# Kernel tuning notes

Hardware: AMD Instinct MI355X
Metric: run time of the kernel (lower is better)

The kernel has to match this reference:

```python
import jax, jax.numpy as jnp
import numpy as np

N_NODES = 100000
N_EDGES = 1600000
IN_CH = 128
HID = 128
OUT_CH = 2
NUM_GRAPHS = 512


def _mlp_params(key, d_in, d_out):
    k1, k2 = jax.random.split(key)
    s1 = 1.0 / np.sqrt(d_in)
    s2 = 1.0 / np.sqrt(d_out)
    return (jax.random.uniform(k1, (d_in, d_out), jnp.float32, -s1, s1),
            jnp.zeros((d_out,), jnp.float32),
            jax.random.uniform(k2, (d_out, d_out), jnp.float32, -s2, s2),
            jnp.zeros((d_out,), jnp.float32))


def setup_inputs() -> dict:
    key = jax.random.key(0)
    ks = jax.random.split(key, 8)
    x = jax.random.normal(ks[0], (N_NODES, IN_CH), jnp.float32)
    edge_index = jax.random.randint(ks[1], (2, N_EDGES), 0, N_NODES, jnp.int64)
    batch = jnp.sort(jax.random.randint(ks[2], (N_NODES,), 0, NUM_GRAPHS, jnp.int64))
    w1_0, b1_0, w2_0, b2_0 = _mlp_params(ks[3], IN_CH, HID)
    w1_1, b1_1, w2_1, b2_1 = _mlp_params(ks[4], HID, HID)
    w1_2, b1_2, w2_2, b2_2 = _mlp_params(ks[5], HID, HID)
    s = 1.0 / np.sqrt(HID)
    w_lin = jax.random.uniform(ks[6], (HID, OUT_CH), jnp.float32, -s, s)
    b_lin = jnp.zeros((OUT_CH,), jnp.float32)
    return {"x": x, "edge_index": edge_index, "batch": batch,
            "w1_0": w1_0, "b1_0": b1_0, "w2_0": w2_0, "b2_0": b2_0,
            "w1_1": w1_1, "b1_1": b1_1, "w2_1": w2_1, "b2_1": b2_1,
            "w1_2": w1_2, "b1_2": b1_2, "w2_2": w2_2, "b2_2": b2_2,
            "w_lin": w_lin, "b_lin": b_lin}


def _gin_conv(x, src, dst, w1, b1, w2, b2):
    # GINConv with eps=0: MLP(x + sum_{j in N(i)} x_j)
    agg = jax.ops.segment_sum(x[src], dst, num_segments=N_NODES)  # [N, d]
    h = x + agg
    h = jax.nn.relu(h @ w1 + b1)
    return h @ w2 + b2


def reference(x, edge_index, batch,
              w1_0, b1_0, w2_0, b2_0,
              w1_1, b1_1, w2_1, b2_1,
              w1_2, b1_2, w2_2, b2_2,
              w_lin, b_lin):
    src, dst = edge_index[0], edge_index[1]
    h = _gin_conv(x, src, dst, w1_0, b1_0, w2_0, b2_0)
    h = jax.nn.relu(h)
    h = jax.nn.relu(_gin_conv(h, src, dst, w1_1, b1_1, w2_1, b2_1))
    h = jax.nn.relu(h)  # forward applies relu twice after GIN1
    h = _gin_conv(h, src, dst, w1_2, b1_2, w2_2, b2_2)
    # global mean pool per graph
    sums = jax.ops.segment_sum(h, batch, num_segments=NUM_GRAPHS)  # [G, d]
    counts = jax.ops.segment_sum(jnp.ones((N_NODES,), h.dtype), batch,
                                 num_segments=NUM_GRAPHS)
    pooled = sums / jnp.maximum(counts, 1.0)[:, None]
    # dropout is identity in eval mode
    return pooled @ w_lin + b_lin  # [G, OUT_CH]
```

## Files before the change

### kernel.cpp

```cpp
#include <hip/hip_runtime.h>
#include <hip/hip_bf16.h>

#define N_NODES   100000
#define N_EDGES   1600000
#define IN_CH     128
#define HID       128
#define OUT_CH    2
#define NUM_GRAPHS 512

#define BKT_SHIFT 9
#define NB2 ((N_NODES + 511) >> BKT_SHIFT)
#define PB  200
#define CHUNK (N_EDGES / PB)

typedef __attribute__((ext_vector_type(8))) short bf16x8;
typedef __attribute__((ext_vector_type(4))) float f32x4;
typedef unsigned int uint32;
typedef unsigned long long uint64;

static __device__ __forceinline__ float b2f(uint32 b) {
    return __uint_as_float(b << 16);
}
static __device__ __forceinline__ unsigned short f2b(float f) {
    uint32 u = __float_as_uint(f);
    u += 0x7fffu + ((u >> 16) & 1u);
    return (unsigned short)(u >> 16);
}
static __device__ __forceinline__ void acc8(float* a, int4 v) {
    uint32 x;
    x = (uint32)v.x; a[0] += __uint_as_float(x << 16); a[1] += __uint_as_float(x & 0xffff0000u);
    x = (uint32)v.y; a[2] += __uint_as_float(x << 16); a[3] += __uint_as_float(x & 0xffff0000u);
    x = (uint32)v.z; a[4] += __uint_as_float(x << 16); a[5] += __uint_as_float(x & 0xffff0000u);
    x = (uint32)v.w; a[6] += __uint_as_float(x << 16); a[7] += __uint_as_float(x & 0xffff0000u);
}

__global__ void k_cast(const float* __restrict__ x, unsigned short* __restrict__ h) {
    int i = blockIdx.x * blockDim.x + threadIdx.x;
    int base = i * 4;
    float4 v = *(const float4*)(x + base);
    ushort4 o;
    o.x = f2b(v.x); o.y = f2b(v.y); o.z = f2b(v.z); o.w = f2b(v.w);
    *(ushort4*)(h + base) = o;
}

__global__ void k_wprep(const float* w0, const float* w1, const float* w2,
                        const float* w3, const float* w4, const float* w5,
                        unsigned short* __restrict__ wt) {
    const float* ws[6] = {w0, w1, w2, w3, w4, w5};
    const float* w = ws[blockIdx.x];
    unsigned short* o = wt + blockIdx.x * 16384;
    for (int i = threadIdx.x; i < 16384; i += 256) {
        int k = i >> 7, n = i & 127;
        o[n * 128 + k] = f2b(w[i]);
    }
}

__global__ void k_p1(const int* __restrict__ dst, int* __restrict__ histG) {
    __shared__ int h[NB2];
    int t = threadIdx.x, blk = blockIdx.x;
    for (int i = t; i < NB2; i += 512) h[i] = 0;
    __syncthreads();
    int base = blk * CHUNK;
    for (int i = t; i < CHUNK; i += 512)
        atomicAdd(&h[dst[base + i] >> BKT_SHIFT], 1);
    __syncthreads();
    for (int i = t; i < NB2; i += 512) histG[i * PB + blk] = h[i];
}

__global__ void k_scan1(const int* __restrict__ in, int* __restrict__ out,
                        int* __restrict__ bsum, int n) {
    __shared__ int sm[256];
    int b = blockIdx.x, t = threadIdx.x;
    int base = b * 1024 + t * 4;
    int v0 = 0, v1 = 0, v2 = 0, v3 = 0;
    if (base + 3 < n) {
        int4 q = *(const int4*)(in + base);
        v0 = q.x; v1 = q.y; v2 = q.z; v3 = q.w;
    } else {
        if (base + 0 < n) v0 = in[base + 0];
        if (base + 1 < n) v1 = in[base + 1];
        if (base + 2 < n) v2 = in[base + 2];
        if (base + 3 < n) v3 = in[base + 3];
    }
    int s = v0 + v1 + v2 + v3;
    sm[t] = s;
    __syncthreads();
    for (int off = 1; off < 256; off <<= 1) {
        int u = (t >= off) ? sm[t - off] : 0;
        __syncthreads();
        sm[t] += u;
        __syncthreads();
    }
    int p = (t == 0) ? 0 : sm[t - 1];
    int o0 = p, o1 = p + v0, o2 = o1 + v1, o3 = o2 + v2;
    if (base + 3 < n) {
        *(int4*)(out + base) = make_int4(o0, o1, o2, o3);
    } else {
        if (base + 0 < n) out[base + 0] = o0;
        if (base + 1 < n) out[base + 1] = o1;
        if (base + 2 < n) out[base + 2] = o2;
        if (base + 3 < n) out[base + 3] = o3;
    }
    if (t == 255) bsum[b] = s + ((t == 0) ? 0 : sm[t - 1]);
}

__global__ void k_scan2(int* __restrict__ bsum, int nb) {
    __shared__ int sm[128];
    int t = threadIdx.x;
    int v = (t < nb) ? bsum[t] : 0;
    sm[t] = v;
    __syncthreads();
    for (int off = 1; off < 128; off <<= 1) {
        int u = (t >= off) ? sm[t - off] : 0;
        __syncthreads();
        sm[t] += u;
        __syncthreads();
    }
    int p = (t == 0) ? 0 : sm[t - 1];
    if (t < nb) bsum[t] = p;
}

__global__ void k_scan3b(int* __restrict__ out, const int* __restrict__ bsum, int n) {
    int b = blockIdx.x, t = threadIdx.x;
    int base = b * 1024 + t * 4;
    int add = bsum[b];
    if (base + 3 < n) {
        int4 q = *(const int4*)(out + base);
        q.x += add; q.y += add; q.z += add; q.w += add;
        *(int4*)(out + base) = q;
    } else {
        for (int j = 0; j < 4; ++j)
            if (base + j < n) out[base + j] += add;
    }
}

__global__ void k_p3(const int* __restrict__ ei, const int* __restrict__ baseG,
                     uint64* __restrict__ ebuf) {
    __shared__ int cur[NB2];
    int t = threadIdx.x, blk = blockIdx.x;
    for (int i = t; i < NB2; i += 512) cur[i] = baseG[i * PB + blk];
    __syncthreads();
    int base = blk * CHUNK;
    for (int i = t; i < CHUNK; i += 512) {
        int e = base + i;
        int src = ei[e];
        int dst = ei[N_EDGES + e];
        int pos = atomicAdd(&cur[dst >> BKT_SHIFT], 1);
        ebuf[pos] = ((uint64)(uint32)dst << 32) | (uint32)src;
    }
}

__global__ void k_p4(const uint64* __restrict__ ebuf, const int* __restrict__ baseG,
                     int* __restrict__ off, int* __restrict__ csr) {
    __shared__ int ldeg[512];
    __shared__ int lscan[512];
    __shared__ int lcur[512];
    int b = blockIdx.x, t = threadIdx.x;
    int node0 = b << BKT_SHIFT;
    int nn = min(512, N_NODES - node0);
    int e0 = baseG[b * PB];
    int e1 = (b == NB2 - 1) ? N_EDGES : baseG[(b + 1) * PB];
    ldeg[t] = 0;
    __syncthreads();
    for (int e = e0 + t; e < e1; e += 512) {
        int dst = (int)(ebuf[e] >> 32);
        atomicAdd(&ldeg[dst - node0], 1);
    }
    __syncthreads();
    lscan[t] = ldeg[t];
    __syncthreads();
    for (int o = 1; o < 512; o <<= 1) {
        int v = (t >= o) ? lscan[t - o] : 0;
        __syncthreads();
        lscan[t] += v;
        __syncthreads();
    }
    int excl = (t == 0) ? 0 : lscan[t - 1];
    lcur[t] = e0 + excl;
    if (t < nn) off[node0 + t] = e0 + excl;
    if (b == NB2 - 1 && t == 0) off[N_NODES] = N_EDGES;
    __syncthreads();
    for (int e = e0 + t; e < e1; e += 512) {
        uint64 pr = ebuf[e];
        int dst = (int)(pr >> 32);
        int pos = atomicAdd(&lcur[dst - node0], 1);
        csr[pos] = (int)(pr & 0xffffffffu);
    }
}

__global__ void k_goff(const int* __restrict__ batch, int* __restrict__ goff) {
    int g = blockIdx.x * blockDim.x + threadIdx.x;
    if (g > NUM_GRAPHS) return;
    int lo = 0, hi = N_NODES;
    while (lo < hi) {
        int mid = (lo + hi) >> 1;
        if (batch[mid] < g) lo = mid + 1; else hi = mid;
    }
    goff[g] = lo;
}

__global__ void k_agg(const unsigned short* __restrict__ h,
                      const int* __restrict__ off, const int* __restrict__ csr,
                      unsigned short* __restrict__ hs) {
    int wid = (blockIdx.x * 256 + threadIdx.x) >> 6;
    int lane = threadIdx.x & 63;
    if (wid >= N_NODES) return;
    int g = lane >> 4, sub = lane & 15;
    int e0 = off[wid], e1 = off[wid + 1];
    float a[8] = {0.f, 0.f, 0.f, 0.f, 0.f, 0.f, 0.f, 0.f};
    int e = e0 + g;
    for (; e + 4 < e1; e += 8) {
        int s0 = csr[e];
        int s1 = csr[e + 4];
        int4 v0 = *(const int4*)(h + (size_t)s0 * 128 + sub * 8);
        int4 v1 = *(const int4*)(h + (size_t)s1 * 128 + sub * 8);
        acc8(a, v0);
        acc8(a, v1);
    }
    if (e < e1) {
        int s0 = csr[e];
        int4 v0 = *(const int4*)(h + (size_t)s0 * 128 + sub * 8);
        acc8(a, v0);
    }
#pragma unroll
    for (int j = 0; j < 8; ++j) {
        a[j] += __shfl_xor(a[j], 16);
        a[j] += __shfl_xor(a[j], 32);
    }
    if (g == 0) {
        int4 sv = *(const int4*)(h + (size_t)wid * 128 + sub * 8);
        acc8(a, sv);
        int4 o;
        o.x = (int)((uint32)f2b(a[0]) | ((uint32)f2b(a[1]) << 16));
        o.y = (int)((uint32)f2b(a[2]) | ((uint32)f2b(a[3]) << 16));
        o.z = (int)((uint32)f2b(a[4]) | ((uint32)f2b(a[5]) << 16));
        o.w = (int)((uint32)f2b(a[6]) | ((uint32)f2b(a[7]) << 16));
        *(int4*)(hs + (size_t)wid * 128 + sub * 8) = o;
    }
}

template<int OUTER_RELU>
__global__ void k_mlp(const unsigned short* __restrict__ hs,
                      const unsigned short* __restrict__ w1t, const float* __restrict__ b1,
                      const unsigned short* __restrict__ w2t, const float* __restrict__ b2,
                      unsigned short* __restrict__ ho) {
    __shared__ unsigned short T[128 * 128];
    int tid = threadIdx.x;
    int lane = tid & 63, wave = tid >> 6;
    int l15 = lane & 15, l4 = lane >> 4;
    int row0 = blockIdx.x * 128;
    int wn0 = wave * 32;

    bf16x8 w1f[2][4], w2f[2][4];
#pragma unroll
    for (int nt = 0; nt < 2; ++nt)
#pragma unroll
        for (int k = 0; k < 4; ++k) {
            int o = (wn0 + nt * 16 + l15) * 128 + k * 32 + l4 * 8;
            w1f[nt][k] = *(const bf16x8*)(w1t + o);
            w2f[nt][k] = *(const bf16x8*)(w2t + o);
        }
    float bias1[2] = { b1[wn0 + l15], b1[wn0 + 16 + l15] };
    float bias2[2] = { b2[wn0 + l15], b2[wn0 + 16 + l15] };

#pragma unroll
    for (int mt = 0; mt < 8; ++mt) {
        int arow = row0 + mt * 16 + l15;
        if (arow >= N_NODES) arow = N_NODES - 1;
        const unsigned short* ap = hs + (size_t)arow * 128 + l4 * 8;
        bf16x8 a0 = *(const bf16x8*)(ap);
        bf16x8 a1 = *(const bf16x8*)(ap + 32);
        bf16x8 a2 = *(const bf16x8*)(ap + 64);
        bf16x8 a3 = *(const bf16x8*)(ap + 96);
#pragma unroll
        for (int nt = 0; nt < 2; ++nt) {
            f32x4 acc = {0.f, 0.f, 0.f, 0.f};
            acc = __builtin_amdgcn_mfma_f32_16x16x32_bf16(a0, w1f[nt][0], acc, 0, 0, 0);
            acc = __builtin_amdgcn_mfma_f32_16x16x32_bf16(a1, w1f[nt][1], acc, 0, 0, 0);
            acc = __builtin_amdgcn_mfma_f32_16x16x32_bf16(a2, w1f[nt][2], acc, 0, 0, 0);
            acc = __builtin_amdgcn_mfma_f32_16x16x32_bf16(a3, w1f[nt][3], acc, 0, 0, 0);
#pragma unroll
            for (int j = 0; j < 4; ++j) {
                float v = fmaxf(acc[j] + bias1[nt], 0.f);
                int trow = mt * 16 + l4 * 4 + j;
                int tcol = wn0 + nt * 16 + l15;
                int byte = (trow * 256 + tcol * 2) ^ ((trow & 7) << 4);
                *(unsigned short*)((char*)T + byte) = f2b(v);
            }
        }
    }
    __syncthreads();

#pragma unroll
    for (int mt = 0; mt < 8; ++mt) {
        int trow = mt * 16 + l15;
        int sw = (trow & 7) << 4;
        int rb = trow * 256 + l4 * 16;
        bf16x8 t0 = *(const bf16x8*)((const char*)T + ((rb + 0)   ^ sw));
        bf16x8 t1 = *(const bf16x8*)((const char*)T + ((rb + 64)  ^ sw));
        bf16x8 t2 = *(const bf16x8*)((const char*)T + ((rb + 128) ^ sw));
        bf16x8 t3 = *(const bf16x8*)((const char*)T + ((rb + 192) ^ sw));
        __syncthreads();
#pragma unroll
        for (int nt = 0; nt < 2; ++nt) {
            f32x4 acc = {0.f, 0.f, 0.f, 0.f};
            acc = __builtin_amdgcn_mfma_f32_16x16x32_bf16(t0, w2f[nt][0], acc, 0, 0, 0);
            acc = __builtin_amdgcn_mfma_f32_16x16x32_bf16(t1, w2f[nt][1], acc, 0, 0, 0);
            acc = __builtin_amdgcn_mfma_f32_16x16x32_bf16(t2, w2f[nt][2], acc, 0, 0, 0);
            acc = __builtin_amdgcn_mfma_f32_16x16x32_bf16(t3, w2f[nt][3], acc, 0, 0, 0);
#pragma unroll
            for (int j = 0; j < 4; ++j) {
                float v = acc[j] + bias2[nt];
                if (OUTER_RELU) v = fmaxf(v, 0.f);
                int orow = mt * 16 + l4 * 4 + j;
                int ocol = wn0 + nt * 16 + l15;
                int byte = (orow * 256 + ocol * 2) ^ ((orow & 7) << 4);
                *(unsigned short*)((char*)T + byte) = f2b(v);
            }
        }
    }
    __syncthreads();

    for (int c = tid; c < 2048; c += 256) {
        int r = c >> 4, cc = c & 15;
        int byte = (r * 256 + cc * 16) ^ ((r & 7) << 4);
        int4 v = *(const int4*)((const char*)T + byte);
        int gr = row0 + r;
        if (gr < N_NODES)
            *(int4*)(ho + (size_t)gr * 128 + cc * 8) = v;
    }
}

__global__ void k_pool(const unsigned short* __restrict__ h,
                       const int* __restrict__ goff,
                       const float* __restrict__ wl, const float* __restrict__ bl,
                       float* __restrict__ out) {
    int g = blockIdx.x;
    int lane = threadIdx.x;
    int e0 = goff[g], e1 = goff[g + 1];
    int c2 = lane << 1;
    float s0 = 0.f, s1 = 0.f;
    int r = e0;
    for (; r + 1 < e1; r += 2) {
        uint32 v0 = *(const uint32*)(h + (size_t)r * 128 + c2);
        uint32 v1 = *(const uint32*)(h + (size_t)(r + 1) * 128 + c2);
        s0 += b2f(v0 & 0xffffu) + b2f(v1 & 0xffffu);
        s1 += b2f(v0 >> 16) + b2f(v1 >> 16);
    }
    if (r < e1) {
        uint32 v = *(const uint32*)(h + (size_t)r * 128 + c2);
        s0 += b2f(v & 0xffffu);
        s1 += b2f(v >> 16);
    }
    float inv = 1.f / fmaxf((float)(e1 - e0), 1.f);
    s0 *= inv; s1 *= inv;
    float o0 = s0 * wl[c2 * 2]     + s1 * wl[(c2 + 1) * 2];
    float o1 = s0 * wl[c2 * 2 + 1] + s1 * wl[(c2 + 1) * 2 + 1];
#pragma unroll
    for (int d = 32; d; d >>= 1) {
        o0 += __shfl_down(o0, d);
        o1 += __shfl_down(o1, d);
    }
    if (lane == 0) {
        out[g * 2]     = o0 + bl[0];
        out[g * 2 + 1] = o1 + bl[1];
    }
}

extern "C" void kernel_launch(void* const* d_in, const int* in_sizes, int n_in,
                              void* d_out, int out_size, void* d_ws, size_t ws_size,
                              hipStream_t stream) {
    const float* x     = (const float*)d_in[0];
    const int*   ei    = (const int*)d_in[1];
    const int*   batch = (const int*)d_in[2];
    const float* w1[3] = {(const float*)d_in[3],  (const float*)d_in[7],  (const float*)d_in[11]};
    const float* b1[3] = {(const float*)d_in[4],  (const float*)d_in[8],  (const float*)d_in[12]};
    const float* w2[3] = {(const float*)d_in[5],  (const float*)d_in[9],  (const float*)d_in[13]};
    const float* b2[3] = {(const float*)d_in[6],  (const float*)d_in[10], (const float*)d_in[14]};
    const float* wl    = (const float*)d_in[15];
    const float* bl    = (const float*)d_in[16];

    char* p = (char*)d_ws;
    auto alloc = [&](size_t bytes) {
        char* r = p;
        p += (bytes + 255) & ~(size_t)255;
        return r;
    };
    int* off    = (int*)alloc((size_t)(N_NODES + 1) * 4);
    int* goff   = (int*)alloc((size_t)(NUM_GRAPHS + 1) * 4);
    int* histG  = (int*)alloc((size_t)(NB2 * PB) * 4);
    int* baseG  = (int*)alloc((size_t)(NB2 * PB + 1) * 4);
    int* bsum   = (int*)alloc((size_t)128 * 4);
    int* csr    = (int*)alloc((size_t)N_EDGES * 4);
    unsigned short* wts = (unsigned short*)alloc((size_t)6 * 16384 * 2);
    unsigned short* hA  = (unsigned short*)alloc((size_t)N_NODES * 128 * 2);
    unsigned short* hS  = (unsigned short*)alloc((size_t)N_NODES * 128 * 2);
    unsigned short* hB  = (unsigned short*)alloc((size_t)N_NODES * 128 * 2);
    uint64* ebuf = (uint64*)hS;

    k_cast<<<(N_NODES * IN_CH / 4 + 255) / 256, 256, 0, stream>>>(x, hA);
    k_wprep<<<6, 256, 0, stream>>>(w1[0], w2[0], w1[1], w2[1], w1[2], w2[2], wts);

    k_p1<<<PB, 512, 0, stream>>>(ei + N_EDGES, histG);
    const int SCAN_N = NB2 * PB;
    const int SCAN_BLOCKS = (SCAN_N + 1023) / 1024;
    k_scan1<<<SCAN_BLOCKS, 256, 0, stream>>>(histG, baseG, bsum, SCAN_N);
    k_scan2<<<1, 128, 0, stream>>>(bsum, SCAN_BLOCKS);
    k_scan3b<<<SCAN_BLOCKS, 256, 0, stream>>>(baseG, bsum, SCAN_N);
    k_p3<<<PB, 512, 0, stream>>>(ei, baseG, ebuf);
    k_p4<<<NB2, 512, 0, stream>>>(ebuf, baseG, off, csr);

    k_goff<<<3, 256, 0, stream>>>(batch, goff);

    unsigned short* wt1[3] = {wts,             wts + 2 * 16384, wts + 4 * 16384};
    unsigned short* wt2[3] = {wts + 1 * 16384, wts + 3 * 16384, wts + 5 * 16384};

    const int AGG_GRID = N_NODES / 4;
    const int MLP_GRID = (N_NODES + 127) / 128;

    k_agg<<<AGG_GRID, 256, 0, stream>>>(hA, off, csr, hS);
    k_mlp<1><<<MLP_GRID, 256, 0, stream>>>(hS, wt1[0], b1[0], wt2[0], b2[0], hB);
    k_agg<<<AGG_GRID, 256, 0, stream>>>(hB, off, csr, hS);
    k_mlp<1><<<MLP_GRID, 256, 0, stream>>>(hS, wt1[1], b1[1], wt2[1], b2[1], hA);
    k_agg<<<AGG_GRID, 256, 0, stream>>>(hA, off, csr, hS);
    k_mlp<0><<<MLP_GRID, 256, 0, stream>>>(hS, wt1[2], b1[2], wt2[2], b2[2], hB);

    k_pool<<<NUM_GRAPHS, 64, 0, stream>>>(hB, goff, wl, bl, (float*)d_out);
}
```

Baseline: 398.1 us.

## Fuse preprocessing launches, unroll gather and pool loops, halve MLP row tile

Merges the cast, weight-prep and histogram kernels into one launch, and folds the graph-offset search into the edge-scatter kernel as extra blocks, removing several launches. The aggregation loop gains a 4-way unrolled stage to keep more neighbour gathers in flight, and the pool loop is unrolled 4-way. The MLP kernel processes 64 rows per block instead of 128, doubling the grid and halving shared memory use to raise occupancy, at the cost of reloading the weight fragments more often. The histogram blocks now run with 256 threads instead of 512.

```diff
diff --git a/kernel.cpp b/kernel.cpp
--- a/kernel.cpp
+++ b/kernel.cpp
@@ -13,6 +13,8 @@
 #define PB  200
 #define CHUNK (N_EDGES / PB)
 
+#define NCAST (N_NODES * IN_CH / 4 / 256)
+
 typedef __attribute__((ext_vector_type(8))) short bf16x8;
 typedef __attribute__((ext_vector_type(4))) float f32x4;
 typedef unsigned int uint32;
@@ -34,37 +36,38 @@
     x = (uint32)v.w; a[6] += __uint_as_float(x << 16); a[7] += __uint_as_float(x & 0xffff0000u);
 }
 
-__global__ void k_cast(const float* __restrict__ x, unsigned short* __restrict__ h) {
-    int i = blockIdx.x * blockDim.x + threadIdx.x;
-    int base = i * 4;
-    float4 v = *(const float4*)(x + base);
-    ushort4 o;
-    o.x = f2b(v.x); o.y = f2b(v.y); o.z = f2b(v.z); o.w = f2b(v.w);
-    *(ushort4*)(h + base) = o;
-}
-
-__global__ void k_wprep(const float* w0, const float* w1, const float* w2,
+__global__ void k_front(const float* __restrict__ x, unsigned short* __restrict__ h,
+                        const float* w0, const float* w1, const float* w2,
                         const float* w3, const float* w4, const float* w5,
-                        unsigned short* __restrict__ wt) {
-    const float* ws[6] = {w0, w1, w2, w3, w4, w5};
-    const float* w = ws[blockIdx.x];
-    unsigned short* o = wt + blockIdx.x * 16384;
-    for (int i = threadIdx.x; i < 16384; i += 256) {
-        int k = i >> 7, n = i & 127;
-        o[n * 128 + k] = f2b(w[i]);
-    }
-}
-
-__global__ void k_p1(const int* __restrict__ dst, int* __restrict__ histG) {
-    __shared__ int h[NB2];
-    int t = threadIdx.x, blk = blockIdx.x;
-    for (int i = t; i < NB2; i += 512) h[i] = 0;
-    __syncthreads();
-    int base = blk * CHUNK;
-    for (int i = t; i < CHUNK; i += 512)
-        atomicAdd(&h[dst[base + i] >> BKT_SHIFT], 1);
-    __syncthreads();
-    for (int i = t; i < NB2; i += 512) histG[i * PB + blk] = h[i];
+                        unsigned short* __restrict__ wt,
+                        const int* __restrict__ dst, int* __restrict__ histG) {
+    __shared__ int hist[NB2];
+    int bid = blockIdx.x, t = threadIdx.x;
+    if (bid < NCAST) {
+        int base = (bid * 256 + t) * 4;
+        float4 v = *(const float4*)(x + base);
+        ushort4 o;
+        o.x = f2b(v.x); o.y = f2b(v.y); o.z = f2b(v.z); o.w = f2b(v.w);
+        *(ushort4*)(h + base) = o;
+    } else if (bid < NCAST + 6) {
+        const float* ws[6] = {w0, w1, w2, w3, w4, w5};
+        int wi = bid - NCAST;
+        const float* w = ws[wi];
+        unsigned short* o = wt + wi * 16384;
+        for (int i = t; i < 16384; i += 256) {
+            int k = i >> 7, n = i & 127;
+            o[n * 128 + k] = f2b(w[i]);
+        }
+    } else {
+        int blk = bid - NCAST - 6;
+        for (int i = t; i < NB2; i += 256) hist[i] = 0;
+        __syncthreads();
+        int base = blk * CHUNK;
+        for (int i = t; i < CHUNK; i += 256)
+            atomicAdd(&hist[dst[base + i] >> BKT_SHIFT], 1);
+        __syncthreads();
+        for (int i = t; i < NB2; i += 256) histG[i * PB + blk] = hist[i];
+    }
 }
 
 __global__ void k_scan1(const int* __restrict__ in, int* __restrict__ out,
@@ -134,10 +137,23 @@
     }
 }
 
-__global__ void k_p3(const int* __restrict__ ei, const int* __restrict__ baseG,
-                     uint64* __restrict__ ebuf) {
+__global__ void k_p3g(const int* __restrict__ ei, const int* __restrict__ baseG,
+                      uint64* __restrict__ ebuf,
+                      const int* __restrict__ batch, int* __restrict__ goff) {
     __shared__ int cur[NB2];
     int t = threadIdx.x, blk = blockIdx.x;
+    if (blk >= PB) {
+        int g = (blk - PB) * 512 + t;
+        if (g <= NUM_GRAPHS) {
+            int lo = 0, hi = N_NODES;
+            while (lo < hi) {
+                int mid = (lo + hi) >> 1;
+                if (batch[mid] < g) lo = mid + 1; else hi = mid;
+            }
+            goff[g] = lo;
+        }
+        return;
+    }
     for (int i = t; i < NB2; i += 512) cur[i] = baseG[i * PB + blk];
     __syncthreads();
     int base = blk * CHUNK;
@@ -188,17 +204,6 @@
     }
 }
 
-__global__ void k_goff(const int* __restrict__ batch, int* __restrict__ goff) {
-    int g = blockIdx.x * blockDim.x + threadIdx.x;
-    if (g > NUM_GRAPHS) return;
-    int lo = 0, hi = N_NODES;
-    while (lo < hi) {
-        int mid = (lo + hi) >> 1;
-        if (batch[mid] < g) lo = mid + 1; else hi = mid;
-    }
-    goff[g] = lo;
-}
-
 __global__ void k_agg(const unsigned short* __restrict__ h,
                       const int* __restrict__ off, const int* __restrict__ csr,
                       unsigned short* __restrict__ hs) {
@@ -209,6 +214,14 @@
     int e0 = off[wid], e1 = off[wid + 1];
     float a[8] = {0.f, 0.f, 0.f, 0.f, 0.f, 0.f, 0.f, 0.f};
     int e = e0 + g;
+    for (; e + 12 < e1; e += 16) {
+        int s0 = csr[e], s1 = csr[e + 4], s2 = csr[e + 8], s3 = csr[e + 12];
+        int4 v0 = *(const int4*)(h + (size_t)s0 * 128 + sub * 8);
+        int4 v1 = *(const int4*)(h + (size_t)s1 * 128 + sub * 8);
+        int4 v2 = *(const int4*)(h + (size_t)s2 * 128 + sub * 8);
+        int4 v3 = *(const int4*)(h + (size_t)s3 * 128 + sub * 8);
+        acc8(a, v0); acc8(a, v1); acc8(a, v2); acc8(a, v3);
+    }
     for (; e + 4 < e1; e += 8) {
         int s0 = csr[e];
         int s1 = csr[e + 4];
@@ -244,11 +257,11 @@
                       const unsigned short* __restrict__ w1t, const float* __restrict__ b1,
                       const unsigned short* __restrict__ w2t, const float* __restrict__ b2,
                       unsigned short* __restrict__ ho) {
-    __shared__ unsigned short T[128 * 128];
+    __shared__ unsigned short T[64 * 128];
     int tid = threadIdx.x;
     int lane = tid & 63, wave = tid >> 6;
     int l15 = lane & 15, l4 = lane >> 4;
-    int row0 = blockIdx.x * 128;
+    int row0 = blockIdx.x * 64;
     int wn0 = wave * 32;
 
     bf16x8 w1f[2][4], w2f[2][4];
@@ -264,7 +277,7 @@
     float bias2[2] = { b2[wn0 + l15], b2[wn0 + 16 + l15] };
 
 #pragma unroll
-    for (int mt = 0; mt < 8; ++mt) {
+    for (int mt = 0; mt < 4; ++mt) {
         int arow = row0 + mt * 16 + l15;
         if (arow >= N_NODES) arow = N_NODES - 1;
         const unsigned short* ap = hs + (size_t)arow * 128 + l4 * 8;
@@ -292,7 +305,7 @@
     __syncthreads();
 
 #pragma unroll
-    for (int mt = 0; mt < 8; ++mt) {
+    for (int mt = 0; mt < 4; ++mt) {
         int trow = mt * 16 + l15;
         int sw = (trow & 7) << 4;
         int rb = trow * 256 + l4 * 16;
@@ -321,7 +334,7 @@
     }
     __syncthreads();
 
-    for (int c = tid; c < 2048; c += 256) {
+    for (int c = tid; c < 1024; c += 256) {
         int r = c >> 4, cc = c & 15;
         int byte = (r * 256 + cc * 16) ^ ((r & 7) << 4);
         int4 v = *(const int4*)((const char*)T + byte);
@@ -341,13 +354,15 @@
     int c2 = lane << 1;
     float s0 = 0.f, s1 = 0.f;
     int r = e0;
-    for (; r + 1 < e1; r += 2) {
+    for (; r + 3 < e1; r += 4) {
         uint32 v0 = *(const uint32*)(h + (size_t)r * 128 + c2);
         uint32 v1 = *(const uint32*)(h + (size_t)(r + 1) * 128 + c2);
-        s0 += b2f(v0 & 0xffffu) + b2f(v1 & 0xffffu);
-        s1 += b2f(v0 >> 16) + b2f(v1 >> 16);
-    }
-    if (r < e1) {
+        uint32 v2 = *(const uint32*)(h + (size_t)(r + 2) * 128 + c2);
+        uint32 v3 = *(const uint32*)(h + (size_t)(r + 3) * 128 + c2);
+        s0 += b2f(v0 & 0xffffu) + b2f(v1 & 0xffffu) + b2f(v2 & 0xffffu) + b2f(v3 & 0xffffu);
+        s1 += b2f(v0 >> 16) + b2f(v1 >> 16) + b2f(v2 >> 16) + b2f(v3 >> 16);
+    }
+    for (; r < e1; ++r) {
         uint32 v = *(const uint32*)(h + (size_t)r * 128 + c2);
         s0 += b2f(v & 0xffffu);
         s1 += b2f(v >> 16);
@@ -398,25 +413,22 @@
     unsigned short* hB  = (unsigned short*)alloc((size_t)N_NODES * 128 * 2);
     uint64* ebuf = (uint64*)hS;
 
-    k_cast<<<(N_NODES * IN_CH / 4 + 255) / 256, 256, 0, stream>>>(x, hA);
-    k_wprep<<<6, 256, 0, stream>>>(w1[0], w2[0], w1[1], w2[1], w1[2], w2[2], wts);
-
-    k_p1<<<PB, 512, 0, stream>>>(ei + N_EDGES, histG);
+    k_front<<<NCAST + 6 + PB, 256, 0, stream>>>(x, hA,
+        w1[0], w2[0], w1[1], w2[1], w1[2], w2[2], wts, ei + N_EDGES, histG);
+
     const int SCAN_N = NB2 * PB;
     const int SCAN_BLOCKS = (SCAN_N + 1023) / 1024;
     k_scan1<<<SCAN_BLOCKS, 256, 0, stream>>>(histG, baseG, bsum, SCAN_N);
     k_scan2<<<1, 128, 0, stream>>>(bsum, SCAN_BLOCKS);
     k_scan3b<<<SCAN_BLOCKS, 256, 0, stream>>>(baseG, bsum, SCAN_N);
-    k_p3<<<PB, 512, 0, stream>>>(ei, baseG, ebuf);
+    k_p3g<<<PB + 2, 512, 0, stream>>>(ei, baseG, ebuf, batch, goff);
     k_p4<<<NB2, 512, 0, stream>>>(ebuf, baseG, off, csr);
-
-    k_goff<<<3, 256, 0, stream>>>(batch, goff);
 
     unsigned short* wt1[3] = {wts,             wts + 2 * 16384, wts + 4 * 16384};
     unsigned short* wt2[3] = {wts + 1 * 16384, wts + 3 * 16384, wts + 5 * 16384};
 
     const int AGG_GRID = N_NODES / 4;
-    const int MLP_GRID = (N_NODES + 127) / 128;
+    const int MLP_GRID = (N_NODES + 63) / 64;
 
     k_agg<<<AGG_GRID, 256, 0, stream>>>(hA, off, csr, hS);
     k_mlp<1><<<MLP_GRID, 256, 0, stream>>>(hS, wt1[0], b1[0], wt2[0], b2[0], hB);
```

Result: faster. 361.5 us (-9.2%).
